# Kernel tuning notes

Measured on AMD Instinct MI355X. Metric: run time of the kernel, lower is better.

## Reference

```python
import jax, jax.numpy as jnp
import numpy as np

B, S, D, H = 2, 2048, 1024, 16
DH = D // H
NEG = jnp.float32(-1e30)


def setup_inputs() -> dict:
    key = jax.random.key(0)
    ks = jax.random.split(key, 5)
    x = jax.random.normal(ks[0], (B, S, D), dtype=jnp.float32)
    # causal mask: attn_mask == 0 means blocked (matches masked_fill(attn_mask == 0))
    attn_mask = jnp.tril(jnp.ones((S, S), dtype=jnp.int32))
    key_padding_mask = jnp.zeros((B, S), dtype=bool)  # True = pad (none here)
    sd = 1.0 / np.sqrt(D)
    W_qkv = jax.random.normal(ks[1], (D, 3 * D), dtype=jnp.float32) * sd
    b_qkv = jnp.zeros((3 * D,), dtype=jnp.float32)
    W_proj = jax.random.normal(ks[2], (D, D), dtype=jnp.float32) * sd
    b_proj = jnp.zeros((D,), dtype=jnp.float32)
    return {"x": x, "W_qkv": W_qkv, "b_qkv": b_qkv, "W_proj": W_proj,
            "b_proj": b_proj, "attn_mask": attn_mask,
            "key_padding_mask": key_padding_mask}


def reference(x, W_qkv, b_qkv, W_proj, b_proj, attn_mask, key_padding_mask):
    scale = jnp.float32(DH) ** -0.5
    qkv = (x @ W_qkv + b_qkv).reshape(B, S, 3, H, DH)
    qkv = jnp.transpose(qkv, (2, 0, 3, 1, 4))  # (3, B, H, S, DH)
    q, k, v = qkv[0], qkv[1], qkv[2]
    attn = jnp.einsum("bhqd,bhkd->bhqk", q, k) * scale  # (B,H,S,S)
    # key padding mask: True -> -inf on that key column
    attn = jnp.where(key_padding_mask[:, None, None, :], NEG, attn)
    # attn mask: 0 -> blocked
    attn = jnp.where(attn_mask[None, None, :, :] == 0, NEG, attn)
    attn = jax.nn.softmax(attn, axis=-1)
    out = jnp.einsum("bhqk,bhkd->bhqd", attn, v)
    out = jnp.transpose(out, (0, 2, 1, 3)).reshape(B, S, D)
    return out @ W_proj + b_proj
```

## Files before the change

### kernel.cpp

```cpp
#include <hip/hip_runtime.h>


typedef __bf16 bf16;
typedef bf16 bf16x4 __attribute__((ext_vector_type(4)));
typedef bf16 bf16x8 __attribute__((ext_vector_type(8)));
typedef float f32x4 __attribute__((ext_vector_type(4)));

#define S_LEN 2048
#define DMODEL 1024
#define NHEAD 16
#define DHEAD 64

__device__ __forceinline__ void async_ld16(void* lds, const void* g) {
  __builtin_amdgcn_global_load_lds(
      (const __attribute__((address_space(1))) unsigned int*)g,
      (__attribute__((address_space(3))) unsigned int*)lds, 16, 0, 0);
}

__global__ __launch_bounds__(256) void prep_kernel(
    const float* __restrict__ x, const float* __restrict__ Wq,
    const float* __restrict__ Wp, bf16* __restrict__ Xb,
    bf16* __restrict__ Wtq, bf16* __restrict__ Wtp) {
  __shared__ float t[32][33];
  const int bid = blockIdx.x, tid = threadIdx.x;
  if (bid < 4096) {
    int i = bid * 256 + tid;
    float4 v = ((const float4*)x)[i];
    bf16x4 o;
    o[0] = (bf16)v.x; o[1] = (bf16)v.y; o[2] = (bf16)v.z; o[3] = (bf16)v.w;
    *(bf16x4*)(&Xb[4 * i]) = o;
    return;
  }
  const float* in; bf16* out; int R, C, bx, by;
  if (bid < 7168) {
    int b = bid - 4096; in = Wq; out = Wtq; R = 1024; C = 3072;
    bx = b % 96; by = b / 96;
  } else {
    int b = bid - 7168; in = Wp; out = Wtp; R = 1024; C = 1024;
    bx = b % 32; by = b / 32;
  }
  int tx = tid & 31, ty = tid >> 5;
  int bc = bx * 32, br = by * 32;
#pragma unroll
  for (int i = 0; i < 32; i += 8)
    t[ty + i][tx] = in[(size_t)(br + ty + i) * C + bc + tx];
  __syncthreads();
#pragma unroll
  for (int i = 0; i < 32; i += 8)
    out[(size_t)(bc + ty + i) * R + br + tx] = (bf16)t[tx][ty + i];
}

__global__ __launch_bounds__(256) void gemm_qkv(
    const bf16* __restrict__ A, const bf16* __restrict__ Bt,
    const float* __restrict__ bias, bf16* __restrict__ Oq,
    bf16* __restrict__ Ok, bf16* __restrict__ Ov, int Ksz) {
  __shared__ bf16 As[2][128 * 32];
  __shared__ bf16 Bs[2][128 * 32];
  const int tid = threadIdx.x, lane = tid & 63, w = tid >> 6;
  const int wm = (w >> 1) * 64, wn = (w & 1) * 64;
  const int lr = lane & 15, kg = lane >> 4;
  const int m0 = blockIdx.y * 128, n0 = blockIdx.x * 128;

  f32x4 acc[4][4] = {};

  bf16x8 areg[2], breg[2];
  const int r0 = tid >> 2,         c0 = (tid & 3) * 8;
  const int r1 = (tid + 256) >> 2, c1 = ((tid + 256) & 3) * 8;

  areg[0] = *(const bf16x8*)(&A[(size_t)(m0 + r0) * Ksz + c0]);
  areg[1] = *(const bf16x8*)(&A[(size_t)(m0 + r1) * Ksz + c1]);
  breg[0] = *(const bf16x8*)(&Bt[(size_t)(n0 + r0) * Ksz + c0]);
  breg[1] = *(const bf16x8*)(&Bt[(size_t)(n0 + r1) * Ksz + c1]);
  *(bf16x8*)(&As[0][r0 * 32 + c0]) = areg[0];
  *(bf16x8*)(&As[0][r1 * 32 + c1]) = areg[1];
  *(bf16x8*)(&Bs[0][r0 * 32 + c0]) = breg[0];
  *(bf16x8*)(&Bs[0][r1 * 32 + c1]) = breg[1];
  areg[0] = *(const bf16x8*)(&A[(size_t)(m0 + r0) * Ksz + 32 + c0]);
  areg[1] = *(const bf16x8*)(&A[(size_t)(m0 + r1) * Ksz + 32 + c1]);
  breg[0] = *(const bf16x8*)(&Bt[(size_t)(n0 + r0) * Ksz + 32 + c0]);
  breg[1] = *(const bf16x8*)(&Bt[(size_t)(n0 + r1) * Ksz + 32 + c1]);
  __syncthreads();

  int cur = 0;
  for (int k0 = 0; k0 < Ksz; k0 += 32) {
    bf16x8 af[4], bfr[4];
#pragma unroll
    for (int i = 0; i < 4; ++i)
      af[i] = *(const bf16x8*)(&As[cur][(wm + i * 16 + lr) * 32 + kg * 8]);
#pragma unroll
    for (int j = 0; j < 4; ++j)
      bfr[j] = *(const bf16x8*)(&Bs[cur][(wn + j * 16 + lr) * 32 + kg * 8]);

    if (k0 + 32 < Ksz) {
      *(bf16x8*)(&As[cur ^ 1][r0 * 32 + c0]) = areg[0];
      *(bf16x8*)(&As[cur ^ 1][r1 * 32 + c1]) = areg[1];
      *(bf16x8*)(&Bs[cur ^ 1][r0 * 32 + c0]) = breg[0];
      *(bf16x8*)(&Bs[cur ^ 1][r1 * 32 + c1]) = breg[1];
      if (k0 + 64 < Ksz) {
        const int kn = k0 + 64;
        areg[0] = *(const bf16x8*)(&A[(size_t)(m0 + r0) * Ksz + kn + c0]);
        areg[1] = *(const bf16x8*)(&A[(size_t)(m0 + r1) * Ksz + kn + c1]);
        breg[0] = *(const bf16x8*)(&Bt[(size_t)(n0 + r0) * Ksz + kn + c0]);
        breg[1] = *(const bf16x8*)(&Bt[(size_t)(n0 + r1) * Ksz + kn + c1]);
      }
    }

#pragma unroll
    for (int i = 0; i < 4; ++i)
#pragma unroll
      for (int j = 0; j < 4; ++j)
        acc[i][j] = __builtin_amdgcn_mfma_f32_16x16x32_bf16(af[i], bfr[j], acc[i][j], 0, 0, 0);
    __syncthreads();
    cur ^= 1;
  }

  const int rbase = kg * 4;
  const int t = n0 >> 10;
  if (t == 2) {
#pragma unroll
    for (int i = 0; i < 4; ++i) {
#pragma unroll
      for (int j = 0; j < 4; ++j) {
        int ncol = n0 + wn + j * 16 + lr;
        float bv = bias[ncol];
        int rem = ncol & 1023, h = rem >> 6, d = rem & 63;
        int m = m0 + wm + i * 16 + rbase;
        int s = m & 2047;
        size_t hb = (size_t)((m >> 11) * NHEAD + h) * S_LEN;
        bf16x4 pk;
#pragma unroll
        for (int r = 0; r < 4; ++r) pk[r] = (bf16)(acc[i][j][r] + bv);
        *(bf16x4*)(&Ov[hb * DHEAD + (size_t)d * S_LEN + s]) = pk;
      }
    }
  } else {
    bf16* Oqk = (t == 0) ? Oq : Ok;
#pragma unroll
    for (int i = 0; i < 4; ++i) {
#pragma unroll
      for (int j = 0; j < 4; ++j) {
        int ncol = n0 + wn + j * 16 + lr;
        float bv = bias[ncol];
        int rem = ncol & 1023, h = rem >> 6, d = rem & 63;
#pragma unroll
        for (int r = 0; r < 4; ++r) {
          int m = m0 + wm + i * 16 + rbase + r;
          int s = m & 2047;
          size_t hb = (size_t)((m >> 11) * NHEAD + h) * S_LEN;
          Oqk[(hb + s) * DHEAD + d] = (bf16)(acc[i][j][r] + bv);
        }
      }
    }
  }
}

__global__ __launch_bounds__(256) void gemm_proj(
    const bf16* __restrict__ A, const bf16* __restrict__ Bt,
    const float* __restrict__ bias, float* __restrict__ Of,
    int Ksz, int Nsz) {
  __shared__ bf16 As[2][64 * 32];
  __shared__ bf16 Bs[2][128 * 32];
  const int tid = threadIdx.x, lane = tid & 63, w = tid >> 6;
  const int wm = (w >> 1) * 32, wn = (w & 1) * 64;
  const int lr = lane & 15, kg = lane >> 4;
  const int m0 = blockIdx.y * 64, n0 = blockIdx.x * 128;

  f32x4 acc[2][4] = {};

  bf16x8 areg, breg[2];
  const int ar_ = tid >> 2,          ac_ = (tid & 3) * 8;
  const int br0 = tid >> 2,          bc0 = (tid & 3) * 8;
  const int br1 = (tid + 256) >> 2,  bc1 = ((tid + 256) & 3) * 8;

  areg    = *(const bf16x8*)(&A[(size_t)(m0 + ar_) * Ksz + ac_]);
  breg[0] = *(const bf16x8*)(&Bt[(size_t)(n0 + br0) * Ksz + bc0]);
  breg[1] = *(const bf16x8*)(&Bt[(size_t)(n0 + br1) * Ksz + bc1]);
  *(bf16x8*)(&As[0][ar_ * 32 + ac_]) = areg;
  *(bf16x8*)(&Bs[0][br0 * 32 + bc0]) = breg[0];
  *(bf16x8*)(&Bs[0][br1 * 32 + bc1]) = breg[1];
  areg    = *(const bf16x8*)(&A[(size_t)(m0 + ar_) * Ksz + 32 + ac_]);
  breg[0] = *(const bf16x8*)(&Bt[(size_t)(n0 + br0) * Ksz + 32 + bc0]);
  breg[1] = *(const bf16x8*)(&Bt[(size_t)(n0 + br1) * Ksz + 32 + bc1]);
  __syncthreads();

  int cur = 0;
  for (int k0 = 0; k0 < Ksz; k0 += 32) {
    bf16x8 af[2], bfr[4];
#pragma unroll
    for (int i = 0; i < 2; ++i)
      af[i] = *(const bf16x8*)(&As[cur][(wm + i * 16 + lr) * 32 + kg * 8]);
#pragma unroll
    for (int j = 0; j < 4; ++j)
      bfr[j] = *(const bf16x8*)(&Bs[cur][(wn + j * 16 + lr) * 32 + kg * 8]);

    if (k0 + 32 < Ksz) {
      *(bf16x8*)(&As[cur ^ 1][ar_ * 32 + ac_]) = areg;
      *(bf16x8*)(&Bs[cur ^ 1][br0 * 32 + bc0]) = breg[0];
      *(bf16x8*)(&Bs[cur ^ 1][br1 * 32 + bc1]) = breg[1];
      if (k0 + 64 < Ksz) {
        const int kn = k0 + 64;
        areg    = *(const bf16x8*)(&A[(size_t)(m0 + ar_) * Ksz + kn + ac_]);
        breg[0] = *(const bf16x8*)(&Bt[(size_t)(n0 + br0) * Ksz + kn + bc0]);
        breg[1] = *(const bf16x8*)(&Bt[(size_t)(n0 + br1) * Ksz + kn + bc1]);
      }
    }

#pragma unroll
    for (int i = 0; i < 2; ++i)
#pragma unroll
      for (int j = 0; j < 4; ++j)
        acc[i][j] = __builtin_amdgcn_mfma_f32_16x16x32_bf16(af[i], bfr[j], acc[i][j], 0, 0, 0);
    __syncthreads();
    cur ^= 1;
  }

  const int rbase = kg * 4;
#pragma unroll
  for (int i = 0; i < 2; ++i) {
#pragma unroll
    for (int j = 0; j < 4; ++j) {
      int ncol = n0 + wn + j * 16 + lr;
      float bv = bias[ncol];
#pragma unroll
      for (int r = 0; r < 4; ++r) {
        int m = m0 + wm + i * 16 + rbase + r;
        Of[(size_t)m * Nsz + ncol] = acc[i][j][r] + bv;
      }
    }
  }
}

__global__ __launch_bounds__(256) void attn_kernel(
    const bf16* __restrict__ Q, const bf16* __restrict__ K,
    const bf16* __restrict__ Vtg, bf16* __restrict__ O) {
  __shared__ bf16 Ks[128 * 72];
  __shared__ bf16 Vt[80 * 136];

  const int tid = threadIdx.x, lane = tid & 63, w = tid >> 6;
  const int lr = lane & 15, quad = lane >> 4;
  const int flat = blockIdx.x;
  const int p = (flat >> 3) & 15;
  const int bh = (flat & 7) + ((flat >> 7) << 3);
  const int b = bh >> 4, h = bh & 15;
  const bf16* Qp = Q + (size_t)bh * S_LEN * DHEAD;
  const bf16* Kp = K + (size_t)bh * S_LEN * DHEAD;
  const bf16* Vp = Vtg + (size_t)bh * S_LEN * DHEAD;

  for (int i = tid; i < 16 * 136; i += 256) {
    int rr = i / 136;
    Vt[(64 + rr) * 136 + (i - rr * 136)] = (rr == 0) ? (bf16)1.0f : (bf16)0.0f;
  }
  __syncthreads();

  const float qs = 0.125f * 1.44269504f;

  for (int seg = 0; seg < 2; ++seg) {
    const int qt = seg ? (31 - p) : p;
    const int q0 = qt * 64;
    const int qrow = q0 + w * 16;

    bf16x8 q0r = *(const bf16x8*)(Qp + (size_t)(qrow + lr) * DHEAD + quad * 8);
    bf16x8 q1r = *(const bf16x8*)(Qp + (size_t)(qrow + lr) * DHEAD + 32 + quad * 8);
    bf16x8 qf0, qf1;
#pragma unroll
    for (int e = 0; e < 8; ++e) {
      qf0[e] = (bf16)((float)q0r[e] * qs);
      qf1[e] = (bf16)((float)q1r[e] * qs);
    }

    f32x4 acc[4] = {};
    f32x4 acc5 = {};

    const int ktiles = (q0 + 63) / 128 + 1;

    bf16x8 kreg[4], vreg[4];
#pragma unroll
    for (int i = 0; i < 4; ++i) {
      int sg = tid + i * 256;
      int krow = sg >> 3, kc = (sg & 7) * 8;
      kreg[i] = *(const bf16x8*)(&Kp[(size_t)krow * DHEAD + kc]);
      int vd = sg >> 4, vs = (sg & 15) * 8;
      vreg[i] = *(const bf16x8*)(&Vp[(size_t)vd * S_LEN + vs]);
    }

    for (int kt = 0; kt < ktiles; ++kt) {
      const int kb = kt * 128;
#pragma unroll
      for (int i = 0; i < 4; ++i) {
        int sg = tid + i * 256;
        int krow = sg >> 3, kc = (sg & 7) * 8;
        int kl = krow & 31;
        int Rrow = (krow & ~31) | (((kl >> 2) & 1) << 4) | (((kl >> 3) & 3) << 2) | (kl & 3);
        *(bf16x8*)(&Ks[Rrow * 72 + kc]) = kreg[i];
        int vd = sg >> 4, vs = (sg & 15) * 8;
        *(bf16x8*)(&Vt[vd * 136 + vs]) = vreg[i];
      }
      __syncthreads();

      if (kt + 1 < ktiles) {
        const int kbn = kb + 128;
#pragma unroll
        for (int i = 0; i < 4; ++i) {
          int sg = tid + i * 256;
          int krow = sg >> 3, kc = (sg & 7) * 8;
          kreg[i] = *(const bf16x8*)(&Kp[(size_t)(kbn + krow) * DHEAD + kc]);
          int vd = sg >> 4, vs = (sg & 15) * 8;
          vreg[i] = *(const bf16x8*)(&Vp[(size_t)vd * S_LEN + kbn + vs]);
        }
      }

      f32x4 sc[8];
      __builtin_amdgcn_s_setprio(1);
#pragma unroll
      for (int ct = 0; ct < 8; ++ct) {
        bf16x8 kf0 = *(const bf16x8*)(&Ks[(ct * 16 + lr) * 72 + quad * 8]);
        bf16x8 kf1 = *(const bf16x8*)(&Ks[(ct * 16 + lr) * 72 + 32 + quad * 8]);
        f32x4 a = {};
        a = __builtin_amdgcn_mfma_f32_16x16x32_bf16(kf0, qf0, a, 0, 0, 0);
        a = __builtin_amdgcn_mfma_f32_16x16x32_bf16(kf1, qf1, a, 0, 0, 0);
        sc[ct] = a;
      }
      __builtin_amdgcn_s_setprio(0);

      if ((kb + 127) > qrow) {
        const int qg = qrow + lr;
#pragma unroll
        for (int ct = 0; ct < 8; ++ct)
#pragma unroll
          for (int r = 0; r < 4; ++r) {
            int key = kb + (ct >> 1) * 32 + quad * 8 + (ct & 1) * 4 + r;
            if (key > qg) sc[ct][r] = -1e30f;
          }
      }

      bf16x8 p8[4];
#pragma unroll
      for (int k0 = 0; k0 < 4; ++k0) {
        bf16x8 pf;
#pragma unroll
        for (int c = 0; c < 2; ++c)
#pragma unroll
          for (int r = 0; r < 4; ++r)
            pf[c * 4 + r] = (bf16)__builtin_amdgcn_exp2f(sc[2 * k0 + c][r]);
        p8[k0] = pf;
      }

      __builtin_amdgcn_s_setprio(1);
#pragma unroll
      for (int k0 = 0; k0 < 4; ++k0) {
#pragma unroll
        for (int nt = 0; nt < 4; ++nt) {
          bf16x8 vf = *(const bf16x8*)(&Vt[(nt * 16 + lr) * 136 + k0 * 32 + quad * 8]);
          acc[nt] = __builtin_amdgcn_mfma_f32_16x16x32_bf16(vf, p8[k0], acc[nt], 0, 0, 0);
        }
        bf16x8 vf5 = *(const bf16x8*)(&Vt[(64 + lr) * 136 + k0 * 32 + quad * 8]);
        acc5 = __builtin_amdgcn_mfma_f32_16x16x32_bf16(vf5, p8[k0], acc5, 0, 0, 0);
      }
      __builtin_amdgcn_s_setprio(0);
      __syncthreads();
    }

    float lsum = __shfl(acc5[0], lr);
    float inv = 1.f / lsum;
    size_t base = ((size_t)(b * S_LEN + qrow + lr)) * DMODEL + h * DHEAD;
#pragma unroll
    for (int nt = 0; nt < 4; ++nt) {
      bf16x4 ov;
#pragma unroll
      for (int r = 0; r < 4; ++r) ov[r] = (bf16)(acc[nt][r] * inv);
      *(bf16x4*)(&O[base + nt * 16 + quad * 4]) = ov;
    }
  }
}

extern "C" void kernel_launch(void* const* d_in, const int* in_sizes, int n_in,
                              void* d_out, int out_size, void* d_ws, size_t ws_size,
                              hipStream_t stream) {
  (void)in_sizes; (void)n_in; (void)out_size; (void)ws_size;
  const float* x     = (const float*)d_in[0];
  const float* Wqkv  = (const float*)d_in[1];
  const float* bqkv  = (const float*)d_in[2];
  const float* Wproj = (const float*)d_in[3];
  const float* bproj = (const float*)d_in[4];
  float* out = (float*)d_out;

  char* ws = (char*)d_ws;
  bf16* Xb  = (bf16*)(ws + 0);
  bf16* AO  = (bf16*)(ws + 0);
  bf16* Wtq = (bf16*)(ws + 8388608);
  bf16* Wtp = (bf16*)(ws + 16777216);
  bf16* Qb  = (bf16*)(ws + 18874368);
  bf16* Kb  = (bf16*)(ws + 27262976);
  bf16* Vtg = (bf16*)(ws + 35651584);

  prep_kernel<<<8192, 256, 0, stream>>>(x, Wqkv, Wproj, Xb, Wtq, Wtp);
  gemm_qkv<<<dim3(24, 32), 256, 0, stream>>>(Xb, Wtq, bqkv, Qb, Kb, Vtg, 1024);
  attn_kernel<<<512, 256, 0, stream>>>(Qb, Kb, Vtg, AO);
  gemm_proj<<<dim3(8, 64), 256, 0, stream>>>(AO, Wtp, bproj, out, 1024, 1024);
}
```

Before: 190.6 us.

## Fuse x bf16 conversion into QKV GEMM and split attention into one tile per block

The separate x-to-bf16 conversion pass is removed. The QKV GEMM now loads fp32 x directly and converts it to bf16 while staging into shared memory, saving a full write and re-read of the activation buffer. The cost is that each GEMM block reads x at twice the bytes, and it is read once per N-tile. Separately, the attention kernel no longer processes two balanced query tiles per block; it launches twice as many blocks with one tile each, using a remapped query-tile order so heavy and light tiles are interleaved for load balance.

```diff
diff --git a/kernel.cpp b/kernel.cpp
--- a/kernel.cpp
+++ b/kernel.cpp
@@ -11,32 +11,24 @@
 #define NHEAD 16
 #define DHEAD 64
 
-__device__ __forceinline__ void async_ld16(void* lds, const void* g) {
-  __builtin_amdgcn_global_load_lds(
-      (const __attribute__((address_space(1))) unsigned int*)g,
-      (__attribute__((address_space(3))) unsigned int*)lds, 16, 0, 0);
+__device__ __forceinline__ bf16x8 cvt8(f32x4 a, f32x4 b) {
+  bf16x8 o;
+#pragma unroll
+  for (int i = 0; i < 4; ++i) { o[i] = (bf16)a[i]; o[4 + i] = (bf16)b[i]; }
+  return o;
 }
 
 __global__ __launch_bounds__(256) void prep_kernel(
-    const float* __restrict__ x, const float* __restrict__ Wq,
-    const float* __restrict__ Wp, bf16* __restrict__ Xb,
+    const float* __restrict__ Wq, const float* __restrict__ Wp,
     bf16* __restrict__ Wtq, bf16* __restrict__ Wtp) {
   __shared__ float t[32][33];
   const int bid = blockIdx.x, tid = threadIdx.x;
-  if (bid < 4096) {
-    int i = bid * 256 + tid;
-    float4 v = ((const float4*)x)[i];
-    bf16x4 o;
-    o[0] = (bf16)v.x; o[1] = (bf16)v.y; o[2] = (bf16)v.z; o[3] = (bf16)v.w;
-    *(bf16x4*)(&Xb[4 * i]) = o;
-    return;
-  }
   const float* in; bf16* out; int R, C, bx, by;
-  if (bid < 7168) {
-    int b = bid - 4096; in = Wq; out = Wtq; R = 1024; C = 3072;
-    bx = b % 96; by = b / 96;
+  if (bid < 3072) {
+    in = Wq; out = Wtq; R = 1024; C = 3072;
+    bx = bid % 96; by = bid / 96;
   } else {
-    int b = bid - 7168; in = Wp; out = Wtp; R = 1024; C = 1024;
+    int b = bid - 3072; in = Wp; out = Wtp; R = 1024; C = 1024;
     bx = b % 32; by = b / 32;
   }
   int tx = tid & 31, ty = tid >> 5;
@@ -51,7 +43,7 @@
 }
 
 __global__ __launch_bounds__(256) void gemm_qkv(
-    const bf16* __restrict__ A, const bf16* __restrict__ Bt,
+    const float* __restrict__ X, const bf16* __restrict__ Bt,
     const float* __restrict__ bias, bf16* __restrict__ Oq,
     bf16* __restrict__ Ok, bf16* __restrict__ Ov, int Ksz) {
   __shared__ bf16 As[2][128 * 32];
@@ -63,20 +55,25 @@
 
   f32x4 acc[4][4] = {};
 
-  bf16x8 areg[2], breg[2];
+  f32x4 xreg[2][2];
+  bf16x8 breg[2];
   const int r0 = tid >> 2,         c0 = (tid & 3) * 8;
   const int r1 = (tid + 256) >> 2, c1 = ((tid + 256) & 3) * 8;
 
-  areg[0] = *(const bf16x8*)(&A[(size_t)(m0 + r0) * Ksz + c0]);
-  areg[1] = *(const bf16x8*)(&A[(size_t)(m0 + r1) * Ksz + c1]);
+  xreg[0][0] = *(const f32x4*)(&X[(size_t)(m0 + r0) * Ksz + c0]);
+  xreg[0][1] = *(const f32x4*)(&X[(size_t)(m0 + r0) * Ksz + c0 + 4]);
+  xreg[1][0] = *(const f32x4*)(&X[(size_t)(m0 + r1) * Ksz + c1]);
+  xreg[1][1] = *(const f32x4*)(&X[(size_t)(m0 + r1) * Ksz + c1 + 4]);
   breg[0] = *(const bf16x8*)(&Bt[(size_t)(n0 + r0) * Ksz + c0]);
   breg[1] = *(const bf16x8*)(&Bt[(size_t)(n0 + r1) * Ksz + c1]);
-  *(bf16x8*)(&As[0][r0 * 32 + c0]) = areg[0];
-  *(bf16x8*)(&As[0][r1 * 32 + c1]) = areg[1];
+  *(bf16x8*)(&As[0][r0 * 32 + c0]) = cvt8(xreg[0][0], xreg[0][1]);
+  *(bf16x8*)(&As[0][r1 * 32 + c1]) = cvt8(xreg[1][0], xreg[1][1]);
   *(bf16x8*)(&Bs[0][r0 * 32 + c0]) = breg[0];
   *(bf16x8*)(&Bs[0][r1 * 32 + c1]) = breg[1];
-  areg[0] = *(const bf16x8*)(&A[(size_t)(m0 + r0) * Ksz + 32 + c0]);
-  areg[1] = *(const bf16x8*)(&A[(size_t)(m0 + r1) * Ksz + 32 + c1]);
+  xreg[0][0] = *(const f32x4*)(&X[(size_t)(m0 + r0) * Ksz + 32 + c0]);
+  xreg[0][1] = *(const f32x4*)(&X[(size_t)(m0 + r0) * Ksz + 32 + c0 + 4]);
+  xreg[1][0] = *(const f32x4*)(&X[(size_t)(m0 + r1) * Ksz + 32 + c1]);
+  xreg[1][1] = *(const f32x4*)(&X[(size_t)(m0 + r1) * Ksz + 32 + c1 + 4]);
   breg[0] = *(const bf16x8*)(&Bt[(size_t)(n0 + r0) * Ksz + 32 + c0]);
   breg[1] = *(const bf16x8*)(&Bt[(size_t)(n0 + r1) * Ksz + 32 + c1]);
   __syncthreads();
@@ -92,14 +89,16 @@
       bfr[j] = *(const bf16x8*)(&Bs[cur][(wn + j * 16 + lr) * 32 + kg * 8]);
 
     if (k0 + 32 < Ksz) {
-      *(bf16x8*)(&As[cur ^ 1][r0 * 32 + c0]) = areg[0];
-      *(bf16x8*)(&As[cur ^ 1][r1 * 32 + c1]) = areg[1];
+      *(bf16x8*)(&As[cur ^ 1][r0 * 32 + c0]) = cvt8(xreg[0][0], xreg[0][1]);
+      *(bf16x8*)(&As[cur ^ 1][r1 * 32 + c1]) = cvt8(xreg[1][0], xreg[1][1]);
       *(bf16x8*)(&Bs[cur ^ 1][r0 * 32 + c0]) = breg[0];
       *(bf16x8*)(&Bs[cur ^ 1][r1 * 32 + c1]) = breg[1];
       if (k0 + 64 < Ksz) {
         const int kn = k0 + 64;
-        areg[0] = *(const bf16x8*)(&A[(size_t)(m0 + r0) * Ksz + kn + c0]);
-        areg[1] = *(const bf16x8*)(&A[(size_t)(m0 + r1) * Ksz + kn + c1]);
+        xreg[0][0] = *(const f32x4*)(&X[(size_t)(m0 + r0) * Ksz + kn + c0]);
+        xreg[0][1] = *(const f32x4*)(&X[(size_t)(m0 + r0) * Ksz + kn + c0 + 4]);
+        xreg[1][0] = *(const f32x4*)(&X[(size_t)(m0 + r1) * Ksz + kn + c1]);
+        xreg[1][1] = *(const f32x4*)(&X[(size_t)(m0 + r1) * Ksz + kn + c1 + 4]);
         breg[0] = *(const bf16x8*)(&Bt[(size_t)(n0 + r0) * Ksz + kn + c0]);
         breg[1] = *(const bf16x8*)(&Bt[(size_t)(n0 + r1) * Ksz + kn + c1]);
       }
@@ -239,8 +238,10 @@
   const int tid = threadIdx.x, lane = tid & 63, w = tid >> 6;
   const int lr = lane & 15, quad = lane >> 4;
   const int flat = blockIdx.x;
-  const int p = (flat >> 3) & 15;
-  const int bh = (flat & 7) + ((flat >> 7) << 3);
+  const int g = (flat >> 3) & 3, t = flat >> 5;
+  const int bh = (flat & 7) + 8 * g;
+  const int qt = (g == 0) ? t : (g == 1) ? (31 - t)
+               : (g == 2) ? ((t + 16) & 31) : ((15 - t) & 31);
   const int b = bh >> 4, h = bh & 15;
   const bf16* Qp = Q + (size_t)bh * S_LEN * DHEAD;
   const bf16* Kp = K + (size_t)bh * S_LEN * DHEAD;
@@ -253,123 +254,119 @@
   __syncthreads();
 
   const float qs = 0.125f * 1.44269504f;
-
-  for (int seg = 0; seg < 2; ++seg) {
-    const int qt = seg ? (31 - p) : p;
-    const int q0 = qt * 64;
-    const int qrow = q0 + w * 16;
-
-    bf16x8 q0r = *(const bf16x8*)(Qp + (size_t)(qrow + lr) * DHEAD + quad * 8);
-    bf16x8 q1r = *(const bf16x8*)(Qp + (size_t)(qrow + lr) * DHEAD + 32 + quad * 8);
-    bf16x8 qf0, qf1;
-#pragma unroll
-    for (int e = 0; e < 8; ++e) {
-      qf0[e] = (bf16)((float)q0r[e] * qs);
-      qf1[e] = (bf16)((float)q1r[e] * qs);
-    }
-
-    f32x4 acc[4] = {};
-    f32x4 acc5 = {};
-
-    const int ktiles = (q0 + 63) / 128 + 1;
-
-    bf16x8 kreg[4], vreg[4];
+  const int q0 = qt * 64;
+  const int qrow = q0 + w * 16;
+
+  bf16x8 q0r = *(const bf16x8*)(Qp + (size_t)(qrow + lr) * DHEAD + quad * 8);
+  bf16x8 q1r = *(const bf16x8*)(Qp + (size_t)(qrow + lr) * DHEAD + 32 + quad * 8);
+  bf16x8 qf0, qf1;
+#pragma unroll
+  for (int e = 0; e < 8; ++e) {
+    qf0[e] = (bf16)((float)q0r[e] * qs);
+    qf1[e] = (bf16)((float)q1r[e] * qs);
+  }
+
+  f32x4 acc[4] = {};
+  f32x4 acc5 = {};
+
+  const int ktiles = (q0 + 63) / 128 + 1;
+
+  bf16x8 kreg[4], vreg[4];
+#pragma unroll
+  for (int i = 0; i < 4; ++i) {
+    int sg = tid + i * 256;
+    int krow = sg >> 3, kc = (sg & 7) * 8;
+    kreg[i] = *(const bf16x8*)(&Kp[(size_t)krow * DHEAD + kc]);
+    int vd = sg >> 4, vs = (sg & 15) * 8;
+    vreg[i] = *(const bf16x8*)(&Vp[(size_t)vd * S_LEN + vs]);
+  }
+
+  for (int kt = 0; kt < ktiles; ++kt) {
+    const int kb = kt * 128;
 #pragma unroll
     for (int i = 0; i < 4; ++i) {
       int sg = tid + i * 256;
       int krow = sg >> 3, kc = (sg & 7) * 8;
-      kreg[i] = *(const bf16x8*)(&Kp[(size_t)krow * DHEAD + kc]);
+      int kl = krow & 31;
+      int Rrow = (krow & ~31) | (((kl >> 2) & 1) << 4) | (((kl >> 3) & 3) << 2) | (kl & 3);
+      *(bf16x8*)(&Ks[Rrow * 72 + kc]) = kreg[i];
       int vd = sg >> 4, vs = (sg & 15) * 8;
-      vreg[i] = *(const bf16x8*)(&Vp[(size_t)vd * S_LEN + vs]);
-    }
-
-    for (int kt = 0; kt < ktiles; ++kt) {
-      const int kb = kt * 128;
+      *(bf16x8*)(&Vt[vd * 136 + vs]) = vreg[i];
+    }
+    __syncthreads();
+
+    if (kt + 1 < ktiles) {
+      const int kbn = kb + 128;
 #pragma unroll
       for (int i = 0; i < 4; ++i) {
         int sg = tid + i * 256;
         int krow = sg >> 3, kc = (sg & 7) * 8;
-        int kl = krow & 31;
-        int Rrow = (krow & ~31) | (((kl >> 2) & 1) << 4) | (((kl >> 3) & 3) << 2) | (kl & 3);
-        *(bf16x8*)(&Ks[Rrow * 72 + kc]) = kreg[i];
+        kreg[i] = *(const bf16x8*)(&Kp[(size_t)(kbn + krow) * DHEAD + kc]);
         int vd = sg >> 4, vs = (sg & 15) * 8;
-        *(bf16x8*)(&Vt[vd * 136 + vs]) = vreg[i];
-      }
-      __syncthreads();
-
-      if (kt + 1 < ktiles) {
-        const int kbn = kb + 128;
-#pragma unroll
-        for (int i = 0; i < 4; ++i) {
-          int sg = tid + i * 256;
-          int krow = sg >> 3, kc = (sg & 7) * 8;
-          kreg[i] = *(const bf16x8*)(&Kp[(size_t)(kbn + krow) * DHEAD + kc]);
-          int vd = sg >> 4, vs = (sg & 15) * 8;
-          vreg[i] = *(const bf16x8*)(&Vp[(size_t)vd * S_LEN + kbn + vs]);
+        vreg[i] = *(const bf16x8*)(&Vp[(size_t)vd * S_LEN + kbn + vs]);
+      }
+    }
+
+    f32x4 sc[8];
+    __builtin_amdgcn_s_setprio(1);
+#pragma unroll
+    for (int ct = 0; ct < 8; ++ct) {
+      bf16x8 kf0 = *(const bf16x8*)(&Ks[(ct * 16 + lr) * 72 + quad * 8]);
+      bf16x8 kf1 = *(const bf16x8*)(&Ks[(ct * 16 + lr) * 72 + 32 + quad * 8]);
+      f32x4 a = {};
+      a = __builtin_amdgcn_mfma_f32_16x16x32_bf16(kf0, qf0, a, 0, 0, 0);
+      a = __builtin_amdgcn_mfma_f32_16x16x32_bf16(kf1, qf1, a, 0, 0, 0);
+      sc[ct] = a;
+    }
+    __builtin_amdgcn_s_setprio(0);
+
+    if ((kb + 127) > qrow) {
+      const int qg = qrow + lr;
+#pragma unroll
+      for (int ct = 0; ct < 8; ++ct)
+#pragma unroll
+        for (int r = 0; r < 4; ++r) {
+          int key = kb + (ct >> 1) * 32 + quad * 8 + (ct & 1) * 4 + r;
+          if (key > qg) sc[ct][r] = -1e30f;
         }
-      }
-
-      f32x4 sc[8];
-      __builtin_amdgcn_s_setprio(1);
-#pragma unroll
-      for (int ct = 0; ct < 8; ++ct) {
-        bf16x8 kf0 = *(const bf16x8*)(&Ks[(ct * 16 + lr) * 72 + quad * 8]);
-        bf16x8 kf1 = *(const bf16x8*)(&Ks[(ct * 16 + lr) * 72 + 32 + quad * 8]);
-        f32x4 a = {};
-        a = __builtin_amdgcn_mfma_f32_16x16x32_bf16(kf0, qf0, a, 0, 0, 0);
-        a = __builtin_amdgcn_mfma_f32_16x16x32_bf16(kf1, qf1, a, 0, 0, 0);
-        sc[ct] = a;
-      }
-      __builtin_amdgcn_s_setprio(0);
-
-      if ((kb + 127) > qrow) {
-        const int qg = qrow + lr;
-#pragma unroll
-        for (int ct = 0; ct < 8; ++ct)
-#pragma unroll
-          for (int r = 0; r < 4; ++r) {
-            int key = kb + (ct >> 1) * 32 + quad * 8 + (ct & 1) * 4 + r;
-            if (key > qg) sc[ct][r] = -1e30f;
-          }
-      }
-
-      bf16x8 p8[4];
-#pragma unroll
-      for (int k0 = 0; k0 < 4; ++k0) {
-        bf16x8 pf;
-#pragma unroll
-        for (int c = 0; c < 2; ++c)
-#pragma unroll
-          for (int r = 0; r < 4; ++r)
-            pf[c * 4 + r] = (bf16)__builtin_amdgcn_exp2f(sc[2 * k0 + c][r]);
-        p8[k0] = pf;
-      }
-
-      __builtin_amdgcn_s_setprio(1);
-#pragma unroll
-      for (int k0 = 0; k0 < 4; ++k0) {
-#pragma unroll
-        for (int nt = 0; nt < 4; ++nt) {
-          bf16x8 vf = *(const bf16x8*)(&Vt[(nt * 16 + lr) * 136 + k0 * 32 + quad * 8]);
-          acc[nt] = __builtin_amdgcn_mfma_f32_16x16x32_bf16(vf, p8[k0], acc[nt], 0, 0, 0);
-        }
-        bf16x8 vf5 = *(const bf16x8*)(&Vt[(64 + lr) * 136 + k0 * 32 + quad * 8]);
-        acc5 = __builtin_amdgcn_mfma_f32_16x16x32_bf16(vf5, p8[k0], acc5, 0, 0, 0);
-      }
-      __builtin_amdgcn_s_setprio(0);
-      __syncthreads();
-    }
-
-    float lsum = __shfl(acc5[0], lr);
-    float inv = 1.f / lsum;
-    size_t base = ((size_t)(b * S_LEN + qrow + lr)) * DMODEL + h * DHEAD;
-#pragma unroll
-    for (int nt = 0; nt < 4; ++nt) {
-      bf16x4 ov;
-#pragma unroll
-      for (int r = 0; r < 4; ++r) ov[r] = (bf16)(acc[nt][r] * inv);
-      *(bf16x4*)(&O[base + nt * 16 + quad * 4]) = ov;
-    }
+    }
+
+    bf16x8 p8[4];
+#pragma unroll
+    for (int k0 = 0; k0 < 4; ++k0) {
+      bf16x8 pf;
+#pragma unroll
+      for (int c = 0; c < 2; ++c)
+#pragma unroll
+        for (int r = 0; r < 4; ++r)
+          pf[c * 4 + r] = (bf16)__builtin_amdgcn_exp2f(sc[2 * k0 + c][r]);
+      p8[k0] = pf;
+    }
+
+    __builtin_amdgcn_s_setprio(1);
+#pragma unroll
+    for (int k0 = 0; k0 < 4; ++k0) {
+#pragma unroll
+      for (int nt = 0; nt < 4; ++nt) {
+        bf16x8 vf = *(const bf16x8*)(&Vt[(nt * 16 + lr) * 136 + k0 * 32 + quad * 8]);
+        acc[nt] = __builtin_amdgcn_mfma_f32_16x16x32_bf16(vf, p8[k0], acc[nt], 0, 0, 0);
+      }
+      bf16x8 vf5 = *(const bf16x8*)(&Vt[(64 + lr) * 136 + k0 * 32 + quad * 8]);
+      acc5 = __builtin_amdgcn_mfma_f32_16x16x32_bf16(vf5, p8[k0], acc5, 0, 0, 0);
+    }
+    __builtin_amdgcn_s_setprio(0);
+    __syncthreads();
+  }
+
+  float lsum = __shfl(acc5[0], lr);
+  float inv = 1.f / lsum;
+  size_t base = ((size_t)(b * S_LEN + qrow + lr)) * DMODEL + h * DHEAD;
+#pragma unroll
+  for (int nt = 0; nt < 4; ++nt) {
+    bf16x4 ov;
+#pragma unroll
+    for (int r = 0; r < 4; ++r) ov[r] = (bf16)(acc[nt][r] * inv);
+    *(bf16x4*)(&O[base + nt * 16 + quad * 4]) = ov;
   }
 }
 
@@ -385,7 +382,6 @@
   float* out = (float*)d_out;
 
   char* ws = (char*)d_ws;
-  bf16* Xb  = (bf16*)(ws + 0);
   bf16* AO  = (bf16*)(ws + 0);
   bf16* Wtq = (bf16*)(ws + 8388608);
   bf16* Wtp = (bf16*)(ws + 16777216);
@@ -393,8 +389,8 @@
   bf16* Kb  = (bf16*)(ws + 27262976);
   bf16* Vtg = (bf16*)(ws + 35651584);
 
-  prep_kernel<<<8192, 256, 0, stream>>>(x, Wqkv, Wproj, Xb, Wtq, Wtp);
-  gemm_qkv<<<dim3(24, 32), 256, 0, stream>>>(Xb, Wtq, bqkv, Qb, Kb, Vtg, 1024);
-  attn_kernel<<<512, 256, 0, stream>>>(Qb, Kb, Vtg, AO);
+  prep_kernel<<<4096, 256, 0, stream>>>(Wqkv, Wproj, Wtq, Wtp);
+  gemm_qkv<<<dim3(24, 32), 256, 0, stream>>>(x, Wtq, bqkv, Qb, Kb, Vtg, 1024);
+  attn_kernel<<<1024, 256, 0, stream>>>(Qb, Kb, Vtg, AO);
   gemm_proj<<<dim3(8, 64), 256, 0, stream>>>(AO, Wtp, bproj, out, 1024, 1024);
 }
```

After: 214.5 us. 12.5% more time.

## Retile QKV GEMM to 256x192 blocks with swizzled LDS and staged prefetch

Applied to the files above, without the earlier changes.

The QKV projection GEMM moves from 128x128 tiles with 4 waves and K-step 32 to 256x192 tiles with 8 waves and K-step 64. The grid drops from 768 to 256 blocks, which matches the number of CUs. LDS rows are XOR-swizzled to avoid bank conflicts. Global prefetch of the next-next tile is spread across four sub-phases, with s_setprio raised around the MFMA bursts. The goal is more data reuse per block and better overlap of loads with MFMA, at the cost of higher register and LDS pressure, extra barriers, and a single wave of blocks.

```diff
diff --git a/kernel.cpp b/kernel.cpp
--- a/kernel.cpp
+++ b/kernel.cpp
@@ -10,12 +10,6 @@
 #define DMODEL 1024
 #define NHEAD 16
 #define DHEAD 64
-
-__device__ __forceinline__ void async_ld16(void* lds, const void* g) {
-  __builtin_amdgcn_global_load_lds(
-      (const __attribute__((address_space(1))) unsigned int*)g,
-      (__attribute__((address_space(3))) unsigned int*)lds, 16, 0, 0);
-}
 
 __global__ __launch_bounds__(256) void prep_kernel(
     const float* __restrict__ x, const float* __restrict__ Wq,
@@ -50,103 +44,124 @@
     out[(size_t)(bc + ty + i) * R + br + tx] = (bf16)t[tx][ty + i];
 }
 
-__global__ __launch_bounds__(256) void gemm_qkv(
+__global__ __launch_bounds__(512, 2) void gemm_qkv(
     const bf16* __restrict__ A, const bf16* __restrict__ Bt,
     const float* __restrict__ bias, bf16* __restrict__ Oq,
     bf16* __restrict__ Ok, bf16* __restrict__ Ov, int Ksz) {
-  __shared__ bf16 As[2][128 * 32];
-  __shared__ bf16 Bs[2][128 * 32];
+  __shared__ bf16 As[2][256 * 64];
+  __shared__ bf16 Bs[2][192 * 64];
   const int tid = threadIdx.x, lane = tid & 63, w = tid >> 6;
-  const int wm = (w >> 1) * 64, wn = (w & 1) * 64;
+  const int wr = w >> 2, wc = w & 3;
+  const int wm = wr * 128, wn = wc * 48;
   const int lr = lane & 15, kg = lane >> 4;
-  const int m0 = blockIdx.y * 128, n0 = blockIdx.x * 128;
-
-  f32x4 acc[4][4] = {};
-
-  bf16x8 areg[2], breg[2];
-  const int r0 = tid >> 2,         c0 = (tid & 3) * 8;
-  const int r1 = (tid + 256) >> 2, c1 = ((tid + 256) & 3) * 8;
-
-  areg[0] = *(const bf16x8*)(&A[(size_t)(m0 + r0) * Ksz + c0]);
-  areg[1] = *(const bf16x8*)(&A[(size_t)(m0 + r1) * Ksz + c1]);
-  breg[0] = *(const bf16x8*)(&Bt[(size_t)(n0 + r0) * Ksz + c0]);
-  breg[1] = *(const bf16x8*)(&Bt[(size_t)(n0 + r1) * Ksz + c1]);
-  *(bf16x8*)(&As[0][r0 * 32 + c0]) = areg[0];
-  *(bf16x8*)(&As[0][r1 * 32 + c1]) = areg[1];
-  *(bf16x8*)(&Bs[0][r0 * 32 + c0]) = breg[0];
-  *(bf16x8*)(&Bs[0][r1 * 32 + c1]) = breg[1];
-  areg[0] = *(const bf16x8*)(&A[(size_t)(m0 + r0) * Ksz + 32 + c0]);
-  areg[1] = *(const bf16x8*)(&A[(size_t)(m0 + r1) * Ksz + 32 + c1]);
-  breg[0] = *(const bf16x8*)(&Bt[(size_t)(n0 + r0) * Ksz + 32 + c0]);
-  breg[1] = *(const bf16x8*)(&Bt[(size_t)(n0 + r1) * Ksz + 32 + c1]);
+  const int m0 = blockIdx.y * 256, n0 = blockIdx.x * 192;
+
+  f32x4 acc[8][3] = {};
+
+  int arow[4], aslot[4], brow[3], bslot[3];
+#pragma unroll
+  for (int c = 0; c < 4; ++c) { int g = tid + c * 512; arow[c] = g >> 3; aslot[c] = g & 7; }
+#pragma unroll
+  for (int c = 0; c < 3; ++c) { int g = tid + c * 512; brow[c] = g >> 3; bslot[c] = g & 7; }
+
+  bf16x8 areg[4], breg[3];
+
+  auto gload = [&](int k0) {
+#pragma unroll
+    for (int c = 0; c < 4; ++c)
+      areg[c] = *(const bf16x8*)(&A[(size_t)(m0 + arow[c]) * Ksz + k0 + aslot[c] * 8]);
+#pragma unroll
+    for (int c = 0; c < 3; ++c)
+      breg[c] = *(const bf16x8*)(&Bt[(size_t)(n0 + brow[c]) * Ksz + k0 + bslot[c] * 8]);
+  };
+  auto swrite = [&](int buf) {
+#pragma unroll
+    for (int c = 0; c < 4; ++c)
+      *(bf16x8*)(&As[buf][arow[c] * 64 + (aslot[c] ^ (arow[c] & 7)) * 8]) = areg[c];
+#pragma unroll
+    for (int c = 0; c < 3; ++c)
+      *(bf16x8*)(&Bs[buf][brow[c] * 64 + (bslot[c] ^ (brow[c] & 7)) * 8]) = breg[c];
+  };
+
+  gload(0);
+  swrite(0);
+  gload(64);
   __syncthreads();
 
-  int cur = 0;
-  for (int k0 = 0; k0 < Ksz; k0 += 32) {
-    bf16x8 af[4], bfr[4];
-#pragma unroll
-    for (int i = 0; i < 4; ++i)
-      af[i] = *(const bf16x8*)(&As[cur][(wm + i * 16 + lr) * 32 + kg * 8]);
-#pragma unroll
-    for (int j = 0; j < 4; ++j)
-      bfr[j] = *(const bf16x8*)(&Bs[cur][(wn + j * 16 + lr) * 32 + kg * 8]);
-
-    if (k0 + 32 < Ksz) {
-      *(bf16x8*)(&As[cur ^ 1][r0 * 32 + c0]) = areg[0];
-      *(bf16x8*)(&As[cur ^ 1][r1 * 32 + c1]) = areg[1];
-      *(bf16x8*)(&Bs[cur ^ 1][r0 * 32 + c0]) = breg[0];
-      *(bf16x8*)(&Bs[cur ^ 1][r1 * 32 + c1]) = breg[1];
-      if (k0 + 64 < Ksz) {
-        const int kn = k0 + 64;
-        areg[0] = *(const bf16x8*)(&A[(size_t)(m0 + r0) * Ksz + kn + c0]);
-        areg[1] = *(const bf16x8*)(&A[(size_t)(m0 + r1) * Ksz + kn + c1]);
-        breg[0] = *(const bf16x8*)(&Bt[(size_t)(n0 + r0) * Ksz + kn + c0]);
-        breg[1] = *(const bf16x8*)(&Bt[(size_t)(n0 + r1) * Ksz + kn + c1]);
-      }
-    }
-
-#pragma unroll
-    for (int i = 0; i < 4; ++i)
-#pragma unroll
-      for (int j = 0; j < 4; ++j)
-        acc[i][j] = __builtin_amdgcn_mfma_f32_16x16x32_bf16(af[i], bfr[j], acc[i][j], 0, 0, 0);
-    __syncthreads();
-    cur ^= 1;
+  const int NT = Ksz >> 6;
+#pragma unroll 1
+  for (int t = 0; t < NT; ++t) {
+    const int cur = t & 1;
+    if (t + 1 < NT) swrite(cur ^ 1);
+    bf16x8 bfr[3];
+#pragma unroll
+    for (int p = 0; p < 4; ++p) {
+      const int kk = p >> 1, ih = (p & 1) * 4;
+      if ((p & 1) == 0) {
+#pragma unroll
+        for (int j = 0; j < 3; ++j) {
+          int row = wn + j * 16 + lr;
+          bfr[j] = *(const bf16x8*)(&Bs[cur][row * 64 + ((kk * 4 + kg) ^ (row & 7)) * 8]);
+        }
+      }
+      bf16x8 af[4];
+#pragma unroll
+      for (int ii = 0; ii < 4; ++ii) {
+        int row = wm + (ih + ii) * 16 + lr;
+        af[ii] = *(const bf16x8*)(&As[cur][row * 64 + ((kk * 4 + kg) ^ (row & 7)) * 8]);
+      }
+      if (t + 2 < NT) {
+        const int kn = (t + 2) << 6;
+        if (p == 0) {
+          areg[0] = *(const bf16x8*)(&A[(size_t)(m0 + arow[0]) * Ksz + kn + aslot[0] * 8]);
+          areg[1] = *(const bf16x8*)(&A[(size_t)(m0 + arow[1]) * Ksz + kn + aslot[1] * 8]);
+        } else if (p == 1) {
+          areg[2] = *(const bf16x8*)(&A[(size_t)(m0 + arow[2]) * Ksz + kn + aslot[2] * 8]);
+          areg[3] = *(const bf16x8*)(&A[(size_t)(m0 + arow[3]) * Ksz + kn + aslot[3] * 8]);
+        } else if (p == 2) {
+          breg[0] = *(const bf16x8*)(&Bt[(size_t)(n0 + brow[0]) * Ksz + kn + bslot[0] * 8]);
+          breg[1] = *(const bf16x8*)(&Bt[(size_t)(n0 + brow[1]) * Ksz + kn + bslot[1] * 8]);
+        } else {
+          breg[2] = *(const bf16x8*)(&Bt[(size_t)(n0 + brow[2]) * Ksz + kn + bslot[2] * 8]);
+        }
+      }
+      __syncthreads();
+      __builtin_amdgcn_s_setprio(1);
+#pragma unroll
+      for (int ii = 0; ii < 4; ++ii)
+#pragma unroll
+        for (int j = 0; j < 3; ++j)
+          acc[ih + ii][j] = __builtin_amdgcn_mfma_f32_16x16x32_bf16(
+              af[ii], bfr[j], acc[ih + ii][j], 0, 0, 0);
+      __builtin_amdgcn_s_setprio(0);
+      __syncthreads();
+    }
   }
 
   const int rbase = kg * 4;
-  const int t = n0 >> 10;
-  if (t == 2) {
-#pragma unroll
-    for (int i = 0; i < 4; ++i) {
-#pragma unroll
-      for (int j = 0; j < 4; ++j) {
-        int ncol = n0 + wn + j * 16 + lr;
-        float bv = bias[ncol];
-        int rem = ncol & 1023, h = rem >> 6, d = rem & 63;
-        int m = m0 + wm + i * 16 + rbase;
+#pragma unroll
+  for (int i = 0; i < 8; ++i) {
+#pragma unroll
+    for (int j = 0; j < 3; ++j) {
+      int ncol = n0 + wn + j * 16 + lr;
+      float bv = bias[ncol];
+      int tt = ncol >> 10, rem = ncol & 1023;
+      int h = rem >> 6, d = rem & 63;
+      int m = m0 + wm + i * 16 + rbase;
+      if (tt == 2) {
         int s = m & 2047;
         size_t hb = (size_t)((m >> 11) * NHEAD + h) * S_LEN;
         bf16x4 pk;
 #pragma unroll
         for (int r = 0; r < 4; ++r) pk[r] = (bf16)(acc[i][j][r] + bv);
         *(bf16x4*)(&Ov[hb * DHEAD + (size_t)d * S_LEN + s]) = pk;
-      }
-    }
-  } else {
-    bf16* Oqk = (t == 0) ? Oq : Ok;
-#pragma unroll
-    for (int i = 0; i < 4; ++i) {
-#pragma unroll
-      for (int j = 0; j < 4; ++j) {
-        int ncol = n0 + wn + j * 16 + lr;
-        float bv = bias[ncol];
-        int rem = ncol & 1023, h = rem >> 6, d = rem & 63;
+      } else {
+        bf16* Oqk = (tt == 0) ? Oq : Ok;
 #pragma unroll
         for (int r = 0; r < 4; ++r) {
-          int m = m0 + wm + i * 16 + rbase + r;
-          int s = m & 2047;
-          size_t hb = (size_t)((m >> 11) * NHEAD + h) * S_LEN;
+          int mm = m + r;
+          int s = mm & 2047;
+          size_t hb = (size_t)((mm >> 11) * NHEAD + h) * S_LEN;
           Oqk[(hb + s) * DHEAD + d] = (bf16)(acc[i][j][r] + bv);
         }
       }
@@ -394,7 +409,7 @@
   bf16* Vtg = (bf16*)(ws + 35651584);
 
   prep_kernel<<<8192, 256, 0, stream>>>(x, Wqkv, Wproj, Xb, Wtq, Wtp);
-  gemm_qkv<<<dim3(24, 32), 256, 0, stream>>>(Xb, Wtq, bqkv, Qb, Kb, Vtg, 1024);
+  gemm_qkv<<<dim3(16, 16), 512, 0, stream>>>(Xb, Wtq, bqkv, Qb, Kb, Vtg, 1024);
   attn_kernel<<<512, 256, 0, stream>>>(Qb, Kb, Vtg, AO);
   gemm_proj<<<dim3(8, 64), 256, 0, stream>>>(AO, Wtp, bproj, out, 1024, 1024);
 }
```

Result: no change. 188.1 us (-1.3%).
